# Kernel tuning notes

Hardware: AMD Instinct MI355X
Metric: run time of the kernel (lower is better)

Reference implementation:

```python
import jax, jax.numpy as jnp
import numpy as np

NU, NI, E, D = 100000, 50000, 600000, 128
NEG_SLOPE = 0.2
EPS = 1e-12


def setup_inputs() -> dict:
    key = jax.random.key(0)
    ks = jax.random.split(key, 10)
    s = 1.0 / np.sqrt(D)  # xavier-ish scale for W
    return {
        "feat_user": jax.random.normal(ks[0], (NU, D), jnp.float32),
        "feat_item": jax.random.normal(ks[1], (NI, D), jnp.float32),
        "norm_user": jax.random.uniform(ks[2], (NU, 1), jnp.float32),
        "norm_item": jax.random.uniform(ks[3], (NI, 1), jnp.float32),
        "norm_ui": jax.random.uniform(ks[4], (E, 1), jnp.float32),
        "norm_iu": jax.random.uniform(ks[5], (E, 1), jnp.float32),
        "W1": jax.random.normal(ks[6], (D, D), jnp.float32) * s,
        "b1": jnp.zeros((D,), jnp.float32),
        "W2": jax.random.normal(ks[7], (D, D), jnp.float32) * s,
        "b2": jnp.zeros((D,), jnp.float32),
        "edge_u": jax.random.randint(ks[8], (E,), 0, NU),
        "edge_i": jax.random.randint(ks[9], (E,), 0, NI),
    }


def _post(h):
    # leaky_relu(0.2) -> dropout (eval: identity) -> row-wise L2 normalize
    h = jnp.where(h > 0, h, NEG_SLOPE * h)
    nrm = jnp.sqrt(jnp.sum(h * h, axis=1, keepdims=True))
    return h / jnp.maximum(nrm, EPS)


def reference(feat_user, feat_item, norm_user, norm_item, norm_ui, norm_iu,
              W1, b1, W2, b2, edge_u, edge_i):
    # edge_message = u_mul_v over ui edges of normed features  [E, D]
    edge_message = (feat_user * norm_user)[edge_u] * (feat_item * norm_item)[edge_i]

    # u_mul_e_sum(iu_g, feat_item, norm_iu): sum_e feat_item[i_e]*norm_iu[e] -> user
    agg_user = jax.ops.segment_sum(feat_item[edge_i] * norm_iu, edge_u, num_segments=NU)
    # u_mul_e_sum(ui_g, feat_user, norm_ui): sum_e feat_user[u_e]*norm_ui[e] -> item
    agg_item = jax.ops.segment_sum(feat_user[edge_u] * norm_ui, edge_i, num_segments=NI)

    # copy_e_sum of edge_message into user (iu dst) and item (ui dst)
    msg_user = jax.ops.segment_sum(edge_message, edge_u, num_segments=NU)
    msg_item = jax.ops.segment_sum(edge_message, edge_i, num_segments=NI)

    h_user = (feat_user + agg_user) @ W1.T + b1 + msg_user @ W2.T + b2
    h_item = (feat_item + agg_item) @ W1.T + b1 + msg_item @ W2.T + b2

    return _post(h_user), _post(h_item)
```

## Files before the change

kernel.cpp:

```cpp
#include <hip/hip_runtime.h>
#include <hip/hip_fp16.h>

#define NU_ 100000
#define NI_ 50000
#define E_  600000
#define DD  128
#define NT_ (NU_ + NI_)

#define BKN 64
#define NBKT ((NT_ + 63) >> 6)
#define SBLK 8192
#define NSB ((E_ + SBLK - 1) / SBLK)
#define NL (NBKT * NSB)
#define NSCB ((NL + 2047) / 2048)
#define MAXE 1024

typedef short bf16x8 __attribute__((ext_vector_type(8)));
typedef float f32x4 __attribute__((ext_vector_type(4)));
typedef unsigned short u16x8 __attribute__((ext_vector_type(8)));

__device__ __forceinline__ unsigned short f2bf(float x) {
  unsigned u = __float_as_uint(x);
  return (unsigned short)((u + 0x7FFFu + ((u >> 16) & 1u)) >> 16);
}
__device__ __forceinline__ float bf2f(unsigned short h) {
  return __uint_as_float((unsigned)h << 16);
}

__device__ __forceinline__ int sidx(int L) {
  int bkt = L / NSB;
  int sb = L - bkt * NSB;
  return sb * NBKT + bkt;
}

__device__ __forceinline__ int swz(int nn, int b) {
  return nn * 256 + (b ^ ((nn & 7) << 4));
}
__device__ __forceinline__ int swz2(int row, int b) {
  return row * 512 + (b ^ ((row & 7) << 4));
}

__global__ __launch_bounds__(256) void pack_kernel(
    const float* __restrict__ W1, const float* __restrict__ W2,
    unsigned short* __restrict__ Bp) {
  int t = blockIdx.x * 256 + threadIdx.x;
  if (t >= 4096) return;
  int w = t >> 11;
  int l = t & 63;
  int kt = (t >> 6) & 3;
  int nt = (t >> 8) & 7;
  const float* W = w ? W2 : W1;
  int n = nt * 16 + (l & 15);
  int k0 = kt * 32 + (l >> 4) * 8;
  unsigned short* dst = Bp + (size_t)t * 8;
#pragma unroll
  for (int j = 0; j < 8; j++) dst[j] = f2bf(W[n * DD + k0 + j]);
}

__global__ __launch_bounds__(256) void tobf_kernel(
    const float* __restrict__ fu, const float* __restrict__ fi,
    unsigned short* __restrict__ fub, unsigned short* __restrict__ fib) {
  int t = blockIdx.x * 256 + threadIdx.x;
  int nu8 = NU_ * DD / 8;
  int nt8 = NT_ * DD / 8;
  if (t >= nt8) return;
  const float* src;
  unsigned short* dst;
  int k;
  if (t < nu8) { src = fu; dst = fub; k = t; }
  else { src = fi; dst = fib; k = t - nu8; }
  const float4 v0 = reinterpret_cast<const float4*>(src)[k * 2];
  const float4 v1 = reinterpret_cast<const float4*>(src)[k * 2 + 1];
  u16x8 o;
  o[0] = f2bf(v0.x); o[1] = f2bf(v0.y); o[2] = f2bf(v0.z); o[3] = f2bf(v0.w);
  o[4] = f2bf(v1.x); o[5] = f2bf(v1.y); o[6] = f2bf(v1.z); o[7] = f2bf(v1.w);
  reinterpret_cast<u16x8*>(dst)[k] = o;
}

__global__ __launch_bounds__(512) void hist_kernel(
    const int* __restrict__ eu, const int* __restrict__ ei, int* __restrict__ hist) {
  __shared__ int cnt[NBKT];
  int sb = blockIdx.x, tid = threadIdx.x;
  for (int k = tid; k < NBKT; k += 512) cnt[k] = 0;
  __syncthreads();
#pragma unroll
  for (int j = 0; j < SBLK / 512; j++) {
    int e = sb * SBLK + j * 512 + tid;
    if (e < E_) {
      atomicAdd(&cnt[eu[e] >> 6], 1);
      atomicAdd(&cnt[(NU_ + ei[e]) >> 6], 1);
    }
  }
  __syncthreads();
  for (int k = tid; k < NBKT; k += 512) hist[sb * NBKT + k] = cnt[k];
}

__global__ __launch_bounds__(256) void scanA_kernel(
    const int* __restrict__ hist, int* __restrict__ off, int* __restrict__ bsum) {
  __shared__ int ts[256];
  int tid = threadIdx.x;
  int base = blockIdx.x * 2048 + tid * 8;
  int v[8];
  int s = 0;
#pragma unroll
  for (int j = 0; j < 8; j++) {
    v[j] = s;
    int L = base + j;
    s += (L < NL) ? hist[sidx(L)] : 0;
  }
  ts[tid] = s;
  __syncthreads();
  for (int ofs = 1; ofs < 256; ofs <<= 1) {
    int add = (tid >= ofs) ? ts[tid - ofs] : 0;
    __syncthreads();
    ts[tid] += add;
    __syncthreads();
  }
  int texcl = ts[tid] - s;
#pragma unroll
  for (int j = 0; j < 8; j++) {
    int L = base + j;
    if (L < NL) off[sidx(L)] = texcl + v[j];
  }
  if (tid == 255) bsum[blockIdx.x] = ts[255];
}

__global__ void scanB_kernel(int* __restrict__ bsum) {
  if (threadIdx.x == 0) {
    int s = 0;
    for (int n = 0; n < NSCB; n++) {
      int t = bsum[n];
      bsum[n] = s;
      s += t;
    }
  }
}

__global__ __launch_bounds__(256) void scanC_kernel(
    int* __restrict__ off, const int* __restrict__ bsum) {
  int L = blockIdx.x * 256 + threadIdx.x;
  if (L >= NL) return;
  off[sidx(L)] += bsum[L >> 11];
}

__global__ __launch_bounds__(512) void scatter_kernel(
    const int* __restrict__ eu, const int* __restrict__ ei,
    const float* __restrict__ nui, const float* __restrict__ niu,
    const int* __restrict__ off, int2* __restrict__ binned) {
  __shared__ int cur[NBKT];
  int sb = blockIdx.x, tid = threadIdx.x;
  for (int k = tid; k < NBKT; k += 512) cur[k] = off[sb * NBKT + k];
  __syncthreads();
#pragma unroll
  for (int j = 0; j < SBLK / 512; j++) {
    int e = sb * SBLK + j * 512 + tid;
    if (e < E_) {
      int u = eu[e], i = ei[e];
      int gi = NU_ + i;
      int s1 = atomicAdd(&cur[u >> 6], 1);
      binned[s1] = make_int2(((u & 63) << 20) | i, __float_as_int(niu[e]));
      int s2 = atomicAdd(&cur[gi >> 6], 1);
      binned[s2] = make_int2(((gi & 63) << 20) | u, __float_as_int(nui[e]));
    }
  }
}

__global__ __launch_bounds__(512, 8) void fused_kernel(
    const unsigned short* __restrict__ fub, const unsigned short* __restrict__ fib,
    const float* __restrict__ nu, const float* __restrict__ ni,
    const int* __restrict__ off, const int2* __restrict__ binned,
    const unsigned short* __restrict__ Bp,
    const float* __restrict__ b1, const float* __restrict__ b2,
    float* __restrict__ out) {
  __shared__ __align__(16) unsigned short XM[2 * BKN * 128];
  __shared__ int eidx[MAXE];
  __shared__ unsigned short ew[MAXE];
  __shared__ int ncnt[BKN];
  __shared__ int nstart[BKN + 1];
  __shared__ int ncur[BKN];
  __shared__ float ssx[BKN][2];

  unsigned short* Xs = XM;
  unsigned short* Ms = XM + BKN * 128;

  int bkt = blockIdx.x, tid = threadIdx.x;
  int bs = off[bkt];
  int be = (bkt + 1 < NBKT) ? off[bkt + 1] : 2 * E_;
  int cnt = be - bs;
  if (cnt > MAXE) cnt = MAXE;

  if (tid < BKN) ncnt[tid] = 0;
  __syncthreads();
  for (int k = tid; k < cnt; k += 512)
    atomicAdd(&ncnt[(binned[bs + k].x >> 20) & 63], 1);
  __syncthreads();

  if (tid < BKN) {
    int a = ncnt[tid];
    int incl = a;
#pragma unroll
    for (int ofs = 1; ofs < 64; ofs <<= 1) {
      int t = __shfl_up(incl, ofs);
      if (tid >= ofs) incl += t;
    }
    if (tid == 0) nstart[0] = 0;
    nstart[tid + 1] = incl;
    ncur[tid] = incl - a;
  }
  __syncthreads();

  for (int k = tid; k < cnt; k += 512) {
    int2 a = binned[bs + k];
    int slot = atomicAdd(&ncur[(a.x >> 20) & 63], 1);
    eidx[slot] = a.x;
    ew[slot] = __half_as_ushort(__float2half(__int_as_float(a.y)));
  }
  __syncthreads();

  int wid = tid >> 6, lane = tid & 63;
  int q = lane >> 4, sub = lane & 15;

  for (int nn = 0; nn < 8; nn++) {
    int gl = wid * 8 + nn;
    int g = bkt * BKN + gl;
    if (g >= NT_) break;
    bool isU = g < NU_;
    const unsigned short* nbF = isU ? fib : fub;
    const float* nbS = isU ? ni : nu;
    int cs = nstart[gl], ce = nstart[gl + 1];

    float aA[8] = {0.f, 0.f, 0.f, 0.f, 0.f, 0.f, 0.f, 0.f};
    float aM[8] = {0.f, 0.f, 0.f, 0.f, 0.f, 0.f, 0.f, 0.f};
    for (int j = cs + q; j < ce; j += 4) {
      int idx = eidx[j] & 0xFFFFF;
      float w = __half2float(__ushort_as_half(ew[j]));
      float snb = nbS[idx];
      u16x8 f = *reinterpret_cast<const u16x8*>(nbF + (size_t)idx * DD + sub * 8);
#pragma unroll
      for (int d = 0; d < 8; d++) {
        float r = bf2f((unsigned short)f[d]);
        aA[d] += r * w;
        aM[d] += r * snb;
      }
    }
#pragma unroll
    for (int d = 0; d < 8; d++) {
      aA[d] += __shfl_xor(aA[d], 16);
      aA[d] += __shfl_xor(aA[d], 32);
      aM[d] += __shfl_xor(aM[d], 16);
      aM[d] += __shfl_xor(aM[d], 32);
    }

    int lrow = isU ? g : g - NU_;
    if (q < 2) {
      const unsigned short* ownp = (isU ? fub : fib) + (size_t)lrow * DD + sub * 8;
      u16x8 fo = *reinterpret_cast<const u16x8*>(ownp);
      u16x8 o;
      if (q == 0) {
#pragma unroll
        for (int d = 0; d < 8; d++)
          o[d] = f2bf(bf2f((unsigned short)fo[d]) + aA[d]);
        *reinterpret_cast<u16x8*>((char*)Xs + swz(gl, sub * 16)) = o;
      } else {
        float so = isU ? nu[lrow] : ni[lrow];
#pragma unroll
        for (int d = 0; d < 8; d++)
          o[d] = f2bf(bf2f((unsigned short)fo[d]) * so * aM[d]);
        *reinterpret_cast<u16x8*>((char*)Ms + swz(gl, sub * 16)) = o;
      }
    }
  }
  __syncthreads();

  int t = wid >> 1, colHalf = wid & 1;
  int gt0 = bkt * BKN + t * 16;
  bool active = gt0 < NT_;

  int lm = lane & 15, lh = lane >> 4;
  float h[4][4];
  float inv4[4];

  if (active) {
    f32x4 acc[4];
#pragma unroll
    for (int nt = 0; nt < 4; nt++) acc[nt] = (f32x4){0.f, 0.f, 0.f, 0.f};

#pragma unroll
    for (int kt = 0; kt < 4; kt++) {
      int b = kt * 64 + lh * 16;
      bf16x8 a1 = *reinterpret_cast<const bf16x8*>((char*)Xs + swz(t * 16 + lm, b));
      bf16x8 a2 = *reinterpret_cast<const bf16x8*>((char*)Ms + swz(t * 16 + lm, b));
#pragma unroll
      for (int nt = 0; nt < 4; nt++) {
        int ntp = colHalf * 4 + nt;
        bf16x8 bf1 = *reinterpret_cast<const bf16x8*>(Bp + ((size_t)((0 * 8 + ntp) * 4 + kt) * 64 + lane) * 8);
        acc[nt] = __builtin_amdgcn_mfma_f32_16x16x32_bf16(a1, bf1, acc[nt], 0, 0, 0);
        bf16x8 bf2 = *reinterpret_cast<const bf16x8*>(Bp + ((size_t)((1 * 8 + ntp) * 4 + kt) * 64 + lane) * 8);
        acc[nt] = __builtin_amdgcn_mfma_f32_16x16x32_bf16(a2, bf2, acc[nt], 0, 0, 0);
      }
    }

    float ss[4] = {0.f, 0.f, 0.f, 0.f};
#pragma unroll
    for (int nt = 0; nt < 4; nt++) {
      int ntp = colHalf * 4 + nt;
      float bb = b1[ntp * 16 + lm] + b2[ntp * 16 + lm];
#pragma unroll
      for (int r = 0; r < 4; r++) {
        float v = acc[nt][r] + bb;
        v = (v > 0.f) ? v : 0.2f * v;
        h[nt][r] = v;
        ss[r] += v * v;
      }
    }
#pragma unroll
    for (int r = 0; r < 4; r++) {
#pragma unroll
      for (int m = 1; m < 16; m <<= 1) ss[r] += __shfl_xor(ss[r], m);
    }
    if (lm == 0) {
#pragma unroll
      for (int r = 0; r < 4; r++) ssx[t * 16 + lh * 4 + r][colHalf] = ss[r];
    }
  }
  __syncthreads();

  if (active) {
#pragma unroll
    for (int r = 0; r < 4; r++) {
      int row = t * 16 + lh * 4 + r;
      float tot = ssx[row][0] + ssx[row][1];
      inv4[r] = 1.0f / fmaxf(sqrtf(tot), 1e-12f);
    }
    float* stg = reinterpret_cast<float*>(XM);
#pragma unroll
    for (int nt = 0; nt < 4; nt++) {
      int ntp = colHalf * 4 + nt;
#pragma unroll
      for (int r = 0; r < 4; r++) {
        int row = t * 16 + lh * 4 + r;
        *reinterpret_cast<float*>((char*)stg + swz2(row, ntp * 64 + lm * 4)) =
            h[nt][r] * inv4[r];
      }
    }
  }
  __syncthreads();

  float* stg = reinterpret_cast<float*>(XM);
  int maxrow = NT_ - bkt * BKN;
  float* ob = out + (size_t)bkt * BKN * DD;
#pragma unroll
  for (int k = 0; k < 4; k++) {
    int c = k * 512 + tid;
    int row = c >> 5;
    if (row < maxrow) {
      f32x4 v = *reinterpret_cast<const f32x4*>((char*)stg + swz2(row, (c & 31) * 16));
      *reinterpret_cast<f32x4*>(ob + (size_t)c * 4) = v;
    }
  }
}

extern "C" void kernel_launch(void* const* d_in, const int* in_sizes, int n_in,
                              void* d_out, int out_size, void* d_ws, size_t ws_size,
                              hipStream_t stream) {
  const float* fu  = (const float*)d_in[0];
  const float* fi  = (const float*)d_in[1];
  const float* nu  = (const float*)d_in[2];
  const float* ni  = (const float*)d_in[3];
  const float* nui = (const float*)d_in[4];
  const float* niu = (const float*)d_in[5];
  const float* W1  = (const float*)d_in[6];
  const float* b1  = (const float*)d_in[7];
  const float* W2  = (const float*)d_in[8];
  const float* b2  = (const float*)d_in[9];
  const int* eu    = (const int*)d_in[10];
  const int* ei    = (const int*)d_in[11];
  float* out = (float*)d_out;
  char* ws = (char*)d_ws;

  size_t off_b = 0;
  auto alloc = [&](size_t bytes) {
    char* p = ws + off_b;
    off_b += (bytes + 255) & ~(size_t)255;
    return p;
  };
  unsigned short* fub = (unsigned short*)alloc((size_t)NU_ * DD * 2);
  unsigned short* fib = (unsigned short*)alloc((size_t)NI_ * DD * 2);
  unsigned short* Bp  = (unsigned short*)alloc(4096 * 8 * 2);
  int* hist = (int*)alloc((size_t)NL * 4);
  int* offc = (int*)alloc((size_t)NL * 4);
  int* bsum = (int*)alloc(256 * 4);
  int2* binned = (int2*)alloc((size_t)2 * E_ * 8);

  pack_kernel<<<16, 256, 0, stream>>>(W1, W2, Bp);
  tobf_kernel<<<(NT_ * DD / 8 + 255) / 256, 256, 0, stream>>>(fu, fi, fub, fib);

  hist_kernel<<<NSB, 512, 0, stream>>>(eu, ei, hist);
  scanA_kernel<<<NSCB, 256, 0, stream>>>(hist, offc, bsum);
  scanB_kernel<<<1, 64, 0, stream>>>(bsum);
  scanC_kernel<<<(NL + 255) / 256, 256, 0, stream>>>(offc, bsum);
  scatter_kernel<<<NSB, 512, 0, stream>>>(eu, ei, nui, niu, offc, binned);

  fused_kernel<<<NBKT, 512, 0, stream>>>(
      fub, fib, nu, ni, offc, binned, Bp, b1, b2, out);
}
```

Baseline: 173.6 us.

## Merge prep kernels, fold scan fixup into consumers, single-pass binned loads

Combines the weight pack, fp32-to-bf16 feature conversion and edge histogram into one launch by dispatching on block index. It drops the separate scan fix-up kernel by adding the block-sum offset where the scatter and fused kernels read offsets. The fused kernel now loads each binned edge once into registers and reuses it for both counting and placement, and it aliases the small shared-memory scratch arrays. Together this cuts three launches and one pass over the binned edge array. The cost is a somewhat heterogeneous prep kernel with 512-thread blocks.

```diff
diff --git a/kernel.cpp b/kernel.cpp
--- a/kernel.cpp
+++ b/kernel.cpp
@@ -15,6 +15,10 @@
 #define NSCB ((NL + 2047) / 2048)
 #define MAXE 1024
 
+#define TOBF_BLKS ((NT_ * DD / 8 + 511) / 512)
+#define PACK_BLKS 8
+#define PREP_BLKS (NSB + TOBF_BLKS + PACK_BLKS)
+
 typedef short bf16x8 __attribute__((ext_vector_type(8)));
 typedef float f32x4 __attribute__((ext_vector_type(4)));
 typedef unsigned short u16x8 __attribute__((ext_vector_type(8)));
@@ -40,10 +44,52 @@
   return row * 512 + (b ^ ((row & 7) << 4));
 }
 
-__global__ __launch_bounds__(256) void pack_kernel(
+__global__ __launch_bounds__(512) void prep_kernel(
+    const float* __restrict__ fu, const float* __restrict__ fi,
     const float* __restrict__ W1, const float* __restrict__ W2,
-    unsigned short* __restrict__ Bp) {
-  int t = blockIdx.x * 256 + threadIdx.x;
+    const int* __restrict__ eu, const int* __restrict__ ei,
+    unsigned short* __restrict__ fub, unsigned short* __restrict__ fib,
+    unsigned short* __restrict__ Bp, int* __restrict__ hist) {
+  __shared__ int cnt[NBKT];
+  int bid = blockIdx.x, tid = threadIdx.x;
+
+  if (bid < NSB) {
+    int sb = bid;
+    for (int k = tid; k < NBKT; k += 512) cnt[k] = 0;
+    __syncthreads();
+#pragma unroll
+    for (int j = 0; j < SBLK / 512; j++) {
+      int e = sb * SBLK + j * 512 + tid;
+      if (e < E_) {
+        atomicAdd(&cnt[eu[e] >> 6], 1);
+        atomicAdd(&cnt[(NU_ + ei[e]) >> 6], 1);
+      }
+    }
+    __syncthreads();
+    for (int k = tid; k < NBKT; k += 512) hist[sb * NBKT + k] = cnt[k];
+    return;
+  }
+
+  if (bid < NSB + TOBF_BLKS) {
+    int t = (bid - NSB) * 512 + tid;
+    int nu8 = NU_ * DD / 8;
+    int nt8 = NT_ * DD / 8;
+    if (t >= nt8) return;
+    const float* src;
+    unsigned short* dst;
+    int k;
+    if (t < nu8) { src = fu; dst = fub; k = t; }
+    else { src = fi; dst = fib; k = t - nu8; }
+    const float4 v0 = reinterpret_cast<const float4*>(src)[k * 2];
+    const float4 v1 = reinterpret_cast<const float4*>(src)[k * 2 + 1];
+    u16x8 o;
+    o[0] = f2bf(v0.x); o[1] = f2bf(v0.y); o[2] = f2bf(v0.z); o[3] = f2bf(v0.w);
+    o[4] = f2bf(v1.x); o[5] = f2bf(v1.y); o[6] = f2bf(v1.z); o[7] = f2bf(v1.w);
+    reinterpret_cast<u16x8*>(dst)[k] = o;
+    return;
+  }
+
+  int t = (bid - NSB - TOBF_BLKS) * 512 + tid;
   if (t >= 4096) return;
   int w = t >> 11;
   int l = t & 63;
@@ -57,44 +103,6 @@
   for (int j = 0; j < 8; j++) dst[j] = f2bf(W[n * DD + k0 + j]);
 }
 
-__global__ __launch_bounds__(256) void tobf_kernel(
-    const float* __restrict__ fu, const float* __restrict__ fi,
-    unsigned short* __restrict__ fub, unsigned short* __restrict__ fib) {
-  int t = blockIdx.x * 256 + threadIdx.x;
-  int nu8 = NU_ * DD / 8;
-  int nt8 = NT_ * DD / 8;
-  if (t >= nt8) return;
-  const float* src;
-  unsigned short* dst;
-  int k;
-  if (t < nu8) { src = fu; dst = fub; k = t; }
-  else { src = fi; dst = fib; k = t - nu8; }
-  const float4 v0 = reinterpret_cast<const float4*>(src)[k * 2];
-  const float4 v1 = reinterpret_cast<const float4*>(src)[k * 2 + 1];
-  u16x8 o;
-  o[0] = f2bf(v0.x); o[1] = f2bf(v0.y); o[2] = f2bf(v0.z); o[3] = f2bf(v0.w);
-  o[4] = f2bf(v1.x); o[5] = f2bf(v1.y); o[6] = f2bf(v1.z); o[7] = f2bf(v1.w);
-  reinterpret_cast<u16x8*>(dst)[k] = o;
-}
-
-__global__ __launch_bounds__(512) void hist_kernel(
-    const int* __restrict__ eu, const int* __restrict__ ei, int* __restrict__ hist) {
-  __shared__ int cnt[NBKT];
-  int sb = blockIdx.x, tid = threadIdx.x;
-  for (int k = tid; k < NBKT; k += 512) cnt[k] = 0;
-  __syncthreads();
-#pragma unroll
-  for (int j = 0; j < SBLK / 512; j++) {
-    int e = sb * SBLK + j * 512 + tid;
-    if (e < E_) {
-      atomicAdd(&cnt[eu[e] >> 6], 1);
-      atomicAdd(&cnt[(NU_ + ei[e]) >> 6], 1);
-    }
-  }
-  __syncthreads();
-  for (int k = tid; k < NBKT; k += 512) hist[sb * NBKT + k] = cnt[k];
-}
-
 __global__ __launch_bounds__(256) void scanA_kernel(
     const int* __restrict__ hist, int* __restrict__ off, int* __restrict__ bsum) {
   __shared__ int ts[256];
@@ -136,20 +144,15 @@
   }
 }
 
-__global__ __launch_bounds__(256) void scanC_kernel(
-    int* __restrict__ off, const int* __restrict__ bsum) {
-  int L = blockIdx.x * 256 + threadIdx.x;
-  if (L >= NL) return;
-  off[sidx(L)] += bsum[L >> 11];
-}
-
 __global__ __launch_bounds__(512) void scatter_kernel(
     const int* __restrict__ eu, const int* __restrict__ ei,
     const float* __restrict__ nui, const float* __restrict__ niu,
-    const int* __restrict__ off, int2* __restrict__ binned) {
+    const int* __restrict__ off, const int* __restrict__ bsum,
+    int2* __restrict__ binned) {
   __shared__ int cur[NBKT];
   int sb = blockIdx.x, tid = threadIdx.x;
-  for (int k = tid; k < NBKT; k += 512) cur[k] = off[sb * NBKT + k];
+  for (int k = tid; k < NBKT; k += 512)
+    cur[k] = off[sb * NBKT + k] + bsum[(k * NSB + sb) >> 11];
   __syncthreads();
 #pragma unroll
   for (int j = 0; j < SBLK / 512; j++) {
@@ -168,31 +171,40 @@
 __global__ __launch_bounds__(512, 8) void fused_kernel(
     const unsigned short* __restrict__ fub, const unsigned short* __restrict__ fib,
     const float* __restrict__ nu, const float* __restrict__ ni,
-    const int* __restrict__ off, const int2* __restrict__ binned,
+    const int* __restrict__ off, const int* __restrict__ bsum,
+    const int2* __restrict__ binned,
     const unsigned short* __restrict__ Bp,
     const float* __restrict__ b1, const float* __restrict__ b2,
     float* __restrict__ out) {
   __shared__ __align__(16) unsigned short XM[2 * BKN * 128];
   __shared__ int eidx[MAXE];
   __shared__ unsigned short ew[MAXE];
-  __shared__ int ncnt[BKN];
+  __shared__ int csrtmp[128];
   __shared__ int nstart[BKN + 1];
-  __shared__ int ncur[BKN];
-  __shared__ float ssx[BKN][2];
 
   unsigned short* Xs = XM;
   unsigned short* Ms = XM + BKN * 128;
+  int* ncnt = csrtmp;
+  int* ncur = csrtmp + 64;
 
   int bkt = blockIdx.x, tid = threadIdx.x;
-  int bs = off[bkt];
-  int be = (bkt + 1 < NBKT) ? off[bkt + 1] : 2 * E_;
+  int bs = off[bkt] + bsum[(bkt * NSB) >> 11];
+  int be = (bkt + 1 < NBKT) ? off[bkt + 1] + bsum[((bkt + 1) * NSB) >> 11] : 2 * E_;
   int cnt = be - bs;
   if (cnt > MAXE) cnt = MAXE;
 
   if (tid < BKN) ncnt[tid] = 0;
   __syncthreads();
-  for (int k = tid; k < cnt; k += 512)
-    atomicAdd(&ncnt[(binned[bs + k].x >> 20) & 63], 1);
+  int2 e0, e1;
+  bool h0 = tid < cnt, h1 = tid + 512 < cnt;
+  if (h0) {
+    e0 = binned[bs + tid];
+    atomicAdd(&ncnt[(e0.x >> 20) & 63], 1);
+  }
+  if (h1) {
+    e1 = binned[bs + tid + 512];
+    atomicAdd(&ncnt[(e1.x >> 20) & 63], 1);
+  }
   __syncthreads();
 
   if (tid < BKN) {
@@ -209,11 +221,15 @@
   }
   __syncthreads();
 
-  for (int k = tid; k < cnt; k += 512) {
-    int2 a = binned[bs + k];
-    int slot = atomicAdd(&ncur[(a.x >> 20) & 63], 1);
-    eidx[slot] = a.x;
-    ew[slot] = __half_as_ushort(__float2half(__int_as_float(a.y)));
+  if (h0) {
+    int slot = atomicAdd(&ncur[(e0.x >> 20) & 63], 1);
+    eidx[slot] = e0.x;
+    ew[slot] = __half_as_ushort(__float2half(__int_as_float(e0.y)));
+  }
+  if (h1) {
+    int slot = atomicAdd(&ncur[(e1.x >> 20) & 63], 1);
+    eidx[slot] = e1.x;
+    ew[slot] = __half_as_ushort(__float2half(__int_as_float(e1.y)));
   }
   __syncthreads();
 
@@ -279,6 +295,7 @@
   int lm = lane & 15, lh = lane >> 4;
   float h[4][4];
   float inv4[4];
+  float (*ssx)[2] = (float(*)[2])csrtmp;
 
   if (active) {
     f32x4 acc[4];
@@ -392,15 +409,12 @@
   int* bsum = (int*)alloc(256 * 4);
   int2* binned = (int2*)alloc((size_t)2 * E_ * 8);
 
-  pack_kernel<<<16, 256, 0, stream>>>(W1, W2, Bp);
-  tobf_kernel<<<(NT_ * DD / 8 + 255) / 256, 256, 0, stream>>>(fu, fi, fub, fib);
-
-  hist_kernel<<<NSB, 512, 0, stream>>>(eu, ei, hist);
+  prep_kernel<<<PREP_BLKS, 512, 0, stream>>>(fu, fi, W1, W2, eu, ei,
+                                             fub, fib, Bp, hist);
   scanA_kernel<<<NSCB, 256, 0, stream>>>(hist, offc, bsum);
   scanB_kernel<<<1, 64, 0, stream>>>(bsum);
-  scanC_kernel<<<(NL + 255) / 256, 256, 0, stream>>>(offc, bsum);
-  scatter_kernel<<<NSB, 512, 0, stream>>>(eu, ei, nui, niu, offc, binned);
+  scatter_kernel<<<NSB, 512, 0, stream>>>(eu, ei, nui, niu, offc, bsum, binned);
 
   fused_kernel<<<NBKT, 512, 0, stream>>>(
-      fub, fib, nu, ni, offc, binned, Bp, b1, b2, out);
-}
+      fub, fib, nu, ni, offc, bsum, binned, Bp, b1, b2, out);
+}
```

After: 166.1 us. -4.3%, faster.
